# Optimization experiments

Hardware: AMD Instinct MI355X
Metric: run time of the kernel (lower is better)

## Reference

```python
import jax, jax.numpy as jnp
import numpy as np

# Config (mirrors MarketBDHConfig / BDHConfig defaults used here)
B, T = 2, 512
NUM_ASSETS, IN_FEAT = 93, 4
D = 256          # n_embd
NH = 4           # n_head
MULT = 64        # mlp_internal_dim_multiplier
NL = 6           # n_layer
NI = D * MULT // NH  # per-head internal dim N = 4096
IN_DIM = NUM_ASSETS * IN_FEAT  # 372
ROPE_THETA = 2.0 ** 16
EPS = 1e-5


def _ln(x):
    # LayerNorm over last dim, elementwise_affine=False
    m = jnp.mean(x, axis=-1, keepdims=True)
    v = jnp.mean(jnp.square(x - m), axis=-1, keepdims=True)
    return (x - m) * jax.lax.rsqrt(v + EPS)


def _rope(x, cos, sin):
    # x: [B,NH,T,NI]; cos/sin: [T, NI//2] (broadcast over B,NH)
    x1, x2 = x[..., 0::2], x[..., 1::2]
    out = jnp.stack([x1 * cos - x2 * sin, x1 * sin + x2 * cos], axis=-1)
    return out.reshape(x.shape)


def setup_inputs() -> dict:
    key = jax.random.key(0)
    ks = jax.random.split(key, 9)
    s = 0.02
    return {
        "x": jax.random.normal(ks[0], (B, T, NUM_ASSETS, IN_FEAT), jnp.float32),
        "in_W": jax.random.normal(ks[1], (IN_DIM, D), jnp.float32) * s,
        "in_b": jnp.zeros((D,), jnp.float32),
        "encoder": jax.random.normal(ks[2], (NH, D, NI), jnp.float32) * s,
        "encoder_v": jax.random.normal(ks[3], (NH, D, NI), jnp.float32) * s,
        "decoder": jax.random.normal(ks[4], (NH * NI, D), jnp.float32) * s,
        "head_W": jax.random.normal(ks[5], (D, IN_DIM), jnp.float32) * s,
        "head_b": jnp.zeros((IN_DIM,), jnp.float32),
    }


def reference(x, in_W, in_b, encoder, encoder_v, decoder, head_W, head_b):
    # input projection: [B,T,N,F] -> [B,T,IN_DIM] -> [B,T,D]
    x_flat = x.reshape(B, T, IN_DIM)
    h = _ln(x_flat @ in_W + in_b)  # [B,T,D]

    # RoPE phase tables over the internal (latent) dimension
    freqs = 1.0 / (ROPE_THETA ** (jnp.arange(0, NI, 2, dtype=jnp.float32) / NI))
    phases = jnp.arange(T, dtype=jnp.float32)[:, None] * freqs[None, :]  # [T, NI/2]
    cos, sin = jnp.cos(phases), jnp.sin(phases)

    dec = decoder.reshape(NH, NI, D)  # head-major flatten matches transpose(1,2).reshape

    for _ in range(NL):
        h_res = h
        # encode + relu-sparsify: [B,NH,T,NI]
        h_sparse = jax.nn.relu(jnp.einsum('btd,hdn->bhtn', h, encoder))
        # BDH attention: linear (no softmax), K is Q, is_causal=False -> dense scores
        qr = _rope(h_sparse, cos, sin)
        scores = jnp.einsum('bhtn,bhsn->bhts', qr, qr)  # [B,NH,T,T]
        yKV = jnp.einsum('bhts,bsd->bhtd', scores, h)    # V = h broadcast over heads
        yKV = _ln(yKV)
        y_sparse = jax.nn.relu(jnp.einsum('bhtd,hdn->bhtn', yKV, encoder_v))
        xy_sparse = h_sparse * y_sparse  # multiplicative gating (dropout p=0)
        yMLP = jnp.einsum('bhtn,hnd->btd', xy_sparse, dec)
        h = _ln(h_res + _ln(yMLP))

    pred = (h @ head_W + head_b).reshape(B, T, NUM_ASSETS, IN_FEAT)
    return pred
```

## Files before the change

kernel.cpp:

```cpp
#include <hip/hip_runtime.h>
#include <math.h>

#define B_ 2
#define T_ 512
#define D_ 256
#define NH_ 4
#define NI_ 4096
#define IN_DIM_ 372
#define NL_ 6
#define EPS_ 1e-5f

typedef unsigned short u16;
typedef __attribute__((ext_vector_type(4))) float f32x4;
typedef __attribute__((ext_vector_type(8))) short bf16x8;

__device__ __forceinline__ u16 f2b(float f) {
  union { float f; unsigned u; } v; v.f = f;
  unsigned r = v.u + 0x7fffu + ((v.u >> 16) & 1u);
  return (u16)(r >> 16);
}
__device__ __forceinline__ float b2f(u16 s) {
  union { unsigned u; float f; } v; v.u = ((unsigned)s) << 16;
  return v.f;
}

__device__ __forceinline__ void gload16(const u16* g, u16* l) {
  __builtin_amdgcn_global_load_lds(
      (const __attribute__((address_space(1))) unsigned int*)g,
      (__attribute__((address_space(3))) unsigned int*)l, 16, 0, 0);
}

__device__ __forceinline__ float waveSum(float v) {
  #pragma unroll
  for (int o = 32; o > 0; o >>= 1) v += __shfl_xor(v, o, 64);
  return v;
}

__device__ __forceinline__ float blkSum256(float v, float* sb4) {
  #pragma unroll
  for (int o = 32; o > 0; o >>= 1) v += __shfl_down(v, o, 64);
  int w = threadIdx.x >> 6;
  __syncthreads();
  if ((threadIdx.x & 63) == 0) sb4[w] = v;
  __syncthreads();
  return sb4[0] + sb4[1] + sb4[2] + sb4[3];
}

__device__ __forceinline__ void gemm128(const u16* __restrict__ A,
                                        const u16* __restrict__ Bt,
                                        int lda, int k0, int k1,
                                        int row0, int col0,
                                        u16* Als, u16* Bls,
                                        f32x4 acc[4][4]) {
  const int tid = threadIdx.x;
  const int lane = tid & 63;
  const int wv = tid >> 6;
  const int wr = (wv >> 1) << 6;
  const int wc = (wv & 1) << 6;
  const int frow = lane & 15;
  const int kg = lane >> 4;
  const int sw = frow & 7;
  #pragma unroll
  for (int m = 0; m < 4; m++)
    #pragma unroll
    for (int n = 0; n < 4; n++) {
      f32x4 z = {0.f, 0.f, 0.f, 0.f};
      acc[m][n] = z;
    }
  auto stage = [&](int k, int buf) {
    #pragma unroll
    for (int i = 0; i < 4; i++) {
      int s = tid + (i << 8);
      int r = s >> 3;
      int c = (((s & 7) ^ (r & 7)) << 3);
      gload16(A + (long)(row0 + r) * lda + k + c, Als + buf * 8192 + s * 8);
      gload16(Bt + (long)(col0 + r) * lda + k + c, Bls + buf * 8192 + s * 8);
    }
  };
  stage(k0, 0);
  __syncthreads();
  int cur = 0;
  for (int k = k0; k < k1; k += 64) {
    if (k + 64 < k1) stage(k + 64, cur ^ 1);
    const u16* Ab = Als + cur * 8192;
    const u16* Bb = Bls + cur * 8192;
    #pragma unroll
    for (int kk = 0; kk < 2; kk++) {
      const int slot = ((((kk << 2) + kg) ^ sw) << 3);
      bf16x8 af[4], bfv[4];
      #pragma unroll
      for (int m = 0; m < 4; m++)
        af[m] = *(const bf16x8*)(Ab + (wr + m * 16 + frow) * 64 + slot);
      #pragma unroll
      for (int n = 0; n < 4; n++)
        bfv[n] = *(const bf16x8*)(Bb + (wc + n * 16 + frow) * 64 + slot);
      #pragma unroll
      for (int m = 0; m < 4; m++)
        #pragma unroll
        for (int n = 0; n < 4; n++)
          acc[m][n] = __builtin_amdgcn_mfma_f32_16x16x32_bf16(af[m], bfv[n], acc[m][n], 0, 0, 0);
    }
    __syncthreads();
    cur ^= 1;
  }
}

#define EPILOG_SETUP \
  const int lane = threadIdx.x & 63; \
  const int wv = threadIdx.x >> 6; \
  const int wr = (wv >> 1) << 6, wc = (wv & 1) << 6;

#define STAGE_HALF(EXPR) \
  if (wr == h * 64) { \
    _Pragma("unroll") \
    for (int m = 0; m < 4; m++) \
      _Pragma("unroll") \
      for (int n = 0; n < 4; n++) \
        _Pragma("unroll") \
        for (int r = 0; r < 4; r++) { \
          int lr = m * 16 + ((lane >> 4) << 2) + r; \
          int lc = wc + n * 16 + (lane & 15); \
          float _a = acc[m][n][r]; \
          smem[lr * 128 + (lc ^ (((lr >> 2) & 7) << 3))] = f2b(EXPR); \
        } \
  } \
  __syncthreads();

__device__ __forceinline__ void storeC_lds(const f32x4 acc[4][4], u16* smem,
                                           u16* Cb, int ldc, int row0, int col0,
                                           int wr, int wc, int lane) {
  const int tid = threadIdx.x;
  #pragma unroll
  for (int h = 0; h < 2; h++) {
    STAGE_HALF(_a)
    #pragma unroll
    for (int i = 0; i < 4; i++) {
      int idx = i * 256 + tid;
      int lr = idx >> 4, ch = idx & 15;
      uint4 v = *(const uint4*)(smem + lr * 128 + ((ch ^ ((lr >> 2) & 7)) << 3));
      *(uint4*)(Cb + (long)(row0 + h * 64 + lr) * ldc + col0 + ch * 8) = v;
    }
    __syncthreads();
  }
}

__global__ __launch_bounds__(256)
void k_cs(unsigned* __restrict__ cs) {
  int idx = blockIdx.x * 256 + threadIdx.x;
  if (idx >= T_ * (NI_ / 2)) return;
  int t = idx >> 11;
  int k = idx & 2047;
  float freq = exp2f(-(float)k * (1.0f / 128.0f));
  float ph = (float)t * freq;
  cs[idx] = (unsigned)f2b(cosf(ph)) | ((unsigned)f2b(sinf(ph)) << 16);
}

__global__ __launch_bounds__(256)
void ktr(const float* __restrict__ src, u16* __restrict__ dst, int R, int C) {
  __shared__ float tile[64][65];
  long zoff = (long)blockIdx.z * R * C;
  int r0 = blockIdx.y * 64, c0 = blockIdx.x * 64;
  int tid = threadIdx.x;
  int tr = tid >> 4, tc4 = (tid & 15) * 4;
  #pragma unroll
  for (int i = 0; i < 4; i++) {
    int r = tr + i * 16;
    f32x4 v = *(const f32x4*)(src + zoff + (long)(r0 + r) * C + c0 + tc4);
    tile[r][tc4 + 0] = v.x; tile[r][tc4 + 1] = v.y;
    tile[r][tc4 + 2] = v.z; tile[r][tc4 + 3] = v.w;
  }
  __syncthreads();
  #pragma unroll
  for (int i = 0; i < 4; i++) {
    int c = tr + i * 16;
    ushort4 o;
    o.x = f2b(tile[tc4 + 0][c]); o.y = f2b(tile[tc4 + 1][c]);
    o.z = f2b(tile[tc4 + 2][c]); o.w = f2b(tile[tc4 + 3][c]);
    *(ushort4*)(dst + zoff + (long)(c0 + c) * R + r0 + tc4) = o;
  }
}

__global__ __launch_bounds__(256)
void ktrW(const float* __restrict__ e0, const float* __restrict__ e1,
          u16* __restrict__ d0, u16* __restrict__ d1) {
  __shared__ float tile[64][65];
  int z = blockIdx.z;
  const float* src = (z < 4) ? e0 : e1;
  u16* dst = (z < 4) ? d0 : d1;
  long zoff = (long)(z & 3) * D_ * NI_;
  int r0 = blockIdx.y * 64, c0 = blockIdx.x * 64;
  int tid = threadIdx.x;
  int tr = tid >> 4, tc4 = (tid & 15) * 4;
  #pragma unroll
  for (int i = 0; i < 4; i++) {
    int r = tr + i * 16;
    f32x4 v = *(const f32x4*)(src + zoff + (long)(r0 + r) * NI_ + c0 + tc4);
    tile[r][tc4 + 0] = v.x; tile[r][tc4 + 1] = v.y;
    tile[r][tc4 + 2] = v.z; tile[r][tc4 + 3] = v.w;
  }
  __syncthreads();
  #pragma unroll
  for (int i = 0; i < 4; i++) {
    int c = tr + i * 16;
    ushort4 o;
    o.x = f2b(tile[tc4 + 0][c]); o.y = f2b(tile[tc4 + 1][c]);
    o.z = f2b(tile[tc4 + 2][c]); o.w = f2b(tile[tc4 + 3][c]);
    *(ushort4*)(dst + zoff + (long)(c0 + c) * D_ + r0 + tc4) = o;
  }
}

__global__ __launch_bounds__(256)
void k_input(const float* __restrict__ x, const float* __restrict__ W,
             const float* __restrict__ b, float* __restrict__ hf,
             u16* __restrict__ hbf, u16* __restrict__ hT) {
  __shared__ float xr[IN_DIM_];
  __shared__ float sb[4];
  int bt = blockIdx.x;
  int d = threadIdx.x;
  const float* xrow = x + (long)bt * IN_DIM_;
  for (int k = d; k < IN_DIM_; k += 256) xr[k] = xrow[k];
  __syncthreads();
  float acc = b[d];
  for (int k = 0; k < IN_DIM_; k++) acc += xr[k] * W[k * D_ + d];
  float mean = blkSum256(acc, sb) * (1.0f / D_);
  float c = acc - mean;
  float var = blkSum256(c * c, sb) * (1.0f / D_);
  float out = c * rsqrtf(var + EPS_);
  hf[(long)bt * D_ + d] = out;
  hbf[(long)bt * D_ + d] = f2b(out);
  hT[((long)(bt >> 9) * D_ + d) * T_ + (bt & 511)] = f2b(out);
}

__global__ __launch_bounds__(256)
void g_enc(const u16* __restrict__ hbf, const u16* __restrict__ enct,
           const unsigned* __restrict__ cs, u16* __restrict__ qr) {
  __shared__ u16 smem[32768];
  int head = blockIdx.z;
  int row0 = blockIdx.y * 128, col0 = blockIdx.x * 128;
  f32x4 acc[4][4];
  gemm128(hbf, enct + (long)head * NI_ * D_, D_, 0, D_, row0, col0,
          smem, smem + 16384, acc);
  EPILOG_SETUP
  const int tid = threadIdx.x;
  #pragma unroll
  for (int h = 0; h < 2; h++) {
    STAGE_HALF(fmaxf(_a, 0.f))
    #pragma unroll
    for (int i = 0; i < 4; i++) {
      int idx = i * 256 + tid;
      int lr = idx >> 4, ch = idx & 15;
      uint4 v = *(const uint4*)(smem + lr * 128 + ((ch ^ ((lr >> 2) & 7)) << 3));
      int gr = row0 + h * 64 + lr;
      int b = gr >> 9, t = gr & 511;
      int gcol = col0 + ch * 8;
      uint4 csv = *(const uint4*)(cs + (long)t * (NI_ / 2) + (gcol >> 1));
      const unsigned* pv = &v.x; const unsigned* pc = &csv.x;
      unsigned o[4];
      #pragma unroll
      for (int j = 0; j < 4; j++) {
        float v0 = b2f((u16)pv[j]), v1 = b2f((u16)(pv[j] >> 16));
        float cc = b2f((u16)pc[j]), ss = b2f((u16)(pc[j] >> 16));
        o[j] = (unsigned)f2b(v0 * cc - v1 * ss) | ((unsigned)f2b(v0 * ss + v1 * cc) << 16);
      }
      long qri = (((long)(b * NH_ + head)) * T_ + t) * NI_ + gcol;
      *(uint4*)(qr + qri) = make_uint4(o[0], o[1], o[2], o[3]);
    }
    __syncthreads();
  }
}

__global__ __launch_bounds__(256)
void g_scores(const u16* __restrict__ qr, u16* __restrict__ scpb) {
  __shared__ u16 smem[32768];
  int tix = blockIdx.x;
  int by = (tix < 4) ? 0 : (tix < 7) ? 1 : (tix < 9) ? 2 : 3;
  int sub = (by == 0) ? 0 : (by == 1) ? 3 : (by == 2) ? 5 : 6;
  int bx = tix - sub;
  int z2 = blockIdx.z;
  int z = z2 >> 2, ks = z2 & 3;
  const u16* A = qr + (long)z * T_ * NI_;
  int row0 = by * 128, col0 = bx * 128;
  f32x4 acc[4][4];
  gemm128(A, A, NI_, ks * 1024, ks * 1024 + 1024, row0, col0,
          smem, smem + 16384, acc);
  EPILOG_SETUP
  u16* Cb = scpb + (long)(ks * 8 + z) * T_ * T_;
  storeC_lds(acc, smem, Cb, T_, row0, col0, wr, wc, lane);
  if (by != bx) {
    #pragma unroll
    for (int m = 0; m < 4; m++)
      #pragma unroll
      for (int n = 0; n < 4; n++) {
        int gc = col0 + wc + n * 16 + (lane & 15);
        int gr0 = row0 + wr + m * 16 + ((lane >> 4) << 2);
        uint2 o;
        o.x = (unsigned)f2b(acc[m][n][0]) | ((unsigned)f2b(acc[m][n][1]) << 16);
        o.y = (unsigned)f2b(acc[m][n][2]) | ((unsigned)f2b(acc[m][n][3]) << 16);
        *(uint2*)(Cb + (long)gc * T_ + gr0) = o;
      }
  }
}

__global__ __launch_bounds__(256)
void g_ykv(const u16* __restrict__ scpb, const u16* __restrict__ hT,
           u16* __restrict__ ykvpb) {
  __shared__ u16 smem[16384];
  u16* Als = smem;
  u16* Bls = smem + 8192;
  int z2 = blockIdx.z;
  int z = z2 >> 2, ks = z2 & 3;
  int b = z >> 2;
  int row0 = blockIdx.y * 128, col0 = blockIdx.x * 128;
  const long SL = (long)8 * T_ * T_;
  const u16* Ab = scpb + (long)z * T_ * T_;
  const u16* Bt = hT + (long)b * D_ * T_;
  const int tid = threadIdx.x;
  const int lane = tid & 63;
  const int wv = tid >> 6;
  const int wr = (wv >> 1) << 6, wc = (wv & 1) << 6;
  const int frow = lane & 15;
  const int kg = lane >> 4;
  const int sw = frow & 7;
  f32x4 acc[4][4];
  #pragma unroll
  for (int m = 0; m < 4; m++)
    #pragma unroll
    for (int n = 0; n < 4; n++) {
      f32x4 zz = {0.f, 0.f, 0.f, 0.f};
      acc[m][n] = zz;
    }
  const int ar = tid >> 1;
  const int ac0 = (tid & 1) << 2;
  for (int k = ks * 128; k < ks * 128 + 128; k += 64) {
    long gb = (long)(row0 + ar) * T_ + k;
    #pragma unroll
    for (int j = 0; j < 4; j++) {
      int jj = ac0 + j;
      long ga = gb + (jj << 3);
      uint4 p0 = *(const uint4*)(Ab + ga);
      uint4 p1 = *(const uint4*)(Ab + SL + ga);
      uint4 p2 = *(const uint4*)(Ab + 2 * SL + ga);
      uint4 p3 = *(const uint4*)(Ab + 3 * SL + ga);
      const unsigned* q0 = &p0.x; const unsigned* q1 = &p1.x;
      const unsigned* q2 = &p2.x; const unsigned* q3 = &p3.x;
      unsigned o[4];
      #pragma unroll
      for (int w = 0; w < 4; w++) {
        float lo = b2f((u16)q0[w]) + b2f((u16)q1[w]) + b2f((u16)q2[w]) + b2f((u16)q3[w]);
        float hi = b2f((u16)(q0[w] >> 16)) + b2f((u16)(q1[w] >> 16)) +
                   b2f((u16)(q2[w] >> 16)) + b2f((u16)(q3[w] >> 16));
        o[w] = (unsigned)f2b(lo) | ((unsigned)f2b(hi) << 16);
      }
      *(uint4*)(Als + ar * 64 + ((jj ^ (ar & 7)) << 3)) = make_uint4(o[0], o[1], o[2], o[3]);
    }
    #pragma unroll
    for (int i = 0; i < 4; i++) {
      int s = tid + (i << 8);
      int r = s >> 3;
      int c = (((s & 7) ^ (r & 7)) << 3);
      gload16(Bt + (long)(col0 + r) * T_ + k + c, Bls + s * 8);
    }
    __syncthreads();
    #pragma unroll
    for (int kk = 0; kk < 2; kk++) {
      const int slot = ((((kk << 2) + kg) ^ sw) << 3);
      bf16x8 af[4], bfv[4];
      #pragma unroll
      for (int m = 0; m < 4; m++)
        af[m] = *(const bf16x8*)(Als + (wr + m * 16 + frow) * 64 + slot);
      #pragma unroll
      for (int n = 0; n < 4; n++)
        bfv[n] = *(const bf16x8*)(Bls + (wc + n * 16 + frow) * 64 + slot);
      #pragma unroll
      for (int m = 0; m < 4; m++)
        #pragma unroll
        for (int n = 0; n < 4; n++)
          acc[m][n] = __builtin_amdgcn_mfma_f32_16x16x32_bf16(af[m], bfv[n], acc[m][n], 0, 0, 0);
    }
    __syncthreads();
  }
  storeC_lds(acc, smem, ykvpb + (long)(ks * 8 + z) * T_ * D_, D_, row0, col0, wr, wc, lane);
}

__global__ __launch_bounds__(256)
void k_lnykv(const u16* __restrict__ ykvpb, u16* __restrict__ ykvb) {
  int row = blockIdx.x * 4 + (threadIdx.x >> 6);
  int lane = threadIdx.x & 63;
  const long SL = (long)8 * T_ * D_;
  long base = (long)row * D_ + lane * 4;
  float v0 = 0.f, v1 = 0.f, v2 = 0.f, v3 = 0.f;
  #pragma unroll
  for (int p = 0; p < 4; p++) {
    uint2 w = *(const uint2*)(ykvpb + p * SL + base);
    v0 += b2f((u16)w.x); v1 += b2f((u16)(w.x >> 16));
    v2 += b2f((u16)w.y); v3 += b2f((u16)(w.y >> 16));
  }
  float mean = waveSum(v0 + v1 + v2 + v3) * (1.0f / D_);
  float c0 = v0 - mean, c1 = v1 - mean, c2 = v2 - mean, c3 = v3 - mean;
  float var = waveSum(c0 * c0 + c1 * c1 + c2 * c2 + c3 * c3) * (1.0f / D_);
  float rs = rsqrtf(var + EPS_);
  uint2 o;
  o.x = (unsigned)f2b(c0 * rs) | ((unsigned)f2b(c1 * rs) << 16);
  o.y = (unsigned)f2b(c2 * rs) | ((unsigned)f2b(c3 * rs) << 16);
  *(uint2*)(ykvb + base) = o;
}

__global__ __launch_bounds__(256)
void g_ysp(const u16* __restrict__ ykvb, const u16* __restrict__ encvt,
           const u16* __restrict__ qr, const unsigned* __restrict__ cs,
           u16* __restrict__ xy) {
  __shared__ u16 smem[32768];
  int z = blockIdx.z;
  int b = z >> 2, head = z & 3;
  int row0 = blockIdx.y * 128, col0 = blockIdx.x * 128;
  f32x4 acc[4][4];
  gemm128(ykvb + (long)z * T_ * D_, encvt + (long)head * NI_ * D_, D_,
          0, D_, row0, col0, smem, smem + 16384, acc);
  EPILOG_SETUP
  const int tid = threadIdx.x;
  #pragma unroll
  for (int h = 0; h < 2; h++) {
    STAGE_HALF(fmaxf(_a, 0.f))
    #pragma unroll
    for (int i = 0; i < 4; i++) {
      int idx = i * 256 + tid;
      int lr = idx >> 4, ch = idx & 15;
      uint4 v = *(const uint4*)(smem + lr * 128 + ((ch ^ ((lr >> 2) & 7)) << 3));
      int t = row0 + h * 64 + lr;
      int gcol = col0 + ch * 8;
      uint4 qv = *(const uint4*)(qr + ((long)z * T_ + t) * NI_ + gcol);
      uint4 csv = *(const uint4*)(cs + (long)t * (NI_ / 2) + (gcol >> 1));
      const unsigned* pv = &v.x; const unsigned* pq = &qv.x; const unsigned* pc = &csv.x;
      unsigned o[4];
      #pragma unroll
      for (int j = 0; j < 4; j++) {
        float v0 = b2f((u16)pv[j]), v1 = b2f((u16)(pv[j] >> 16));
        float q0 = b2f((u16)pq[j]), q1 = b2f((u16)(pq[j] >> 16));
        float cc = b2f((u16)pc[j]), ss = b2f((u16)(pc[j] >> 16));
        float hs0 = fmaxf(cc * q0 + ss * q1, 0.f);
        float hs1 = fmaxf(cc * q1 - ss * q0, 0.f);
        o[j] = (unsigned)f2b(hs0 * v0) | ((unsigned)f2b(hs1 * v1) << 16);
      }
      long xyi = ((long)b * T_ + t) * (NH_ * NI_) + head * NI_ + gcol;
      *(uint4*)(xy + xyi) = make_uint4(o[0], o[1], o[2], o[3]);
    }
    __syncthreads();
  }
}

__global__ __launch_bounds__(256)
void g_ymlp(const u16* __restrict__ xy, const u16* __restrict__ dect,
            u16* __restrict__ ymlppb) {
  __shared__ u16 smem[32768];
  int ks = blockIdx.z;
  int row0 = blockIdx.y * 128, col0 = blockIdx.x * 128;
  f32x4 acc[4][4];
  gemm128(xy, dect, NH_ * NI_, ks * 1024, ks * 1024 + 1024, row0, col0,
          smem, smem + 16384, acc);
  EPILOG_SETUP
  storeC_lds(acc, smem, ymlppb + (long)ks * (B_ * T_) * D_, D_, row0, col0, wr, wc, lane);
}

__global__ __launch_bounds__(256)
void k_dln(const u16* __restrict__ ymlppb, float* __restrict__ hf,
           u16* __restrict__ hbf, u16* __restrict__ hT) {
  int bt = blockIdx.x * 4 + (threadIdx.x >> 6);
  int lane = threadIdx.x & 63;
  const long SL = (long)(B_ * T_) * D_;
  long base = (long)bt * D_ + lane * 4;
  float v0 = 0.f, v1 = 0.f, v2 = 0.f, v3 = 0.f;
  #pragma unroll
  for (int p = 0; p < 16; p++) {
    uint2 w = *(const uint2*)(ymlppb + p * SL + base);
    v0 += b2f((u16)w.x); v1 += b2f((u16)(w.x >> 16));
    v2 += b2f((u16)w.y); v3 += b2f((u16)(w.y >> 16));
  }
  float mean = waveSum(v0 + v1 + v2 + v3) * (1.0f / D_);
  float c0 = v0 - mean, c1 = v1 - mean, c2 = v2 - mean, c3 = v3 - mean;
  float var = waveSum(c0 * c0 + c1 * c1 + c2 * c2 + c3 * c3) * (1.0f / D_);
  float rs = rsqrtf(var + EPS_);
  f32x4 hv = *(const f32x4*)(hf + base);
  float w0 = hv.x + c0 * rs, w1 = hv.y + c1 * rs;
  float w2 = hv.z + c2 * rs, w3 = hv.w + c3 * rs;
  float m2 = waveSum(w0 + w1 + w2 + w3) * (1.0f / D_);
  float e0 = w0 - m2, e1 = w1 - m2, e2 = w2 - m2, e3 = w3 - m2;
  float va2 = waveSum(e0 * e0 + e1 * e1 + e2 * e2 + e3 * e3) * (1.0f / D_);
  float rs2 = rsqrtf(va2 + EPS_);
  float o0 = e0 * rs2, o1 = e1 * rs2, o2 = e2 * rs2, o3 = e3 * rs2;
  f32x4 of = {o0, o1, o2, o3};
  *(f32x4*)(hf + base) = of;
  uint2 ob;
  ob.x = (unsigned)f2b(o0) | ((unsigned)f2b(o1) << 16);
  ob.y = (unsigned)f2b(o2) | ((unsigned)f2b(o3) << 16);
  *(uint2*)(hbf + base) = ob;
  int b = bt >> 9, t = bt & 511;
  int d0 = lane * 4;
  hT[((long)b * D_ + d0 + 0) * T_ + t] = f2b(o0);
  hT[((long)b * D_ + d0 + 1) * T_ + t] = f2b(o1);
  hT[((long)b * D_ + d0 + 2) * T_ + t] = f2b(o2);
  hT[((long)b * D_ + d0 + 3) * T_ + t] = f2b(o3);
}

__global__ __launch_bounds__(384)
void k_head(const float* __restrict__ h, const float* __restrict__ W,
            const float* __restrict__ bb, float* __restrict__ out) {
  __shared__ float hr[D_];
  int bt = blockIdx.x;
  int j = threadIdx.x;
  for (int k = j; k < D_; k += 384) hr[k] = h[(long)bt * D_ + k];
  __syncthreads();
  if (j < IN_DIM_) {
    float acc = bb[j];
    for (int d2 = 0; d2 < D_; d2++) acc += hr[d2] * W[(long)d2 * IN_DIM_ + j];
    out[(long)bt * IN_DIM_ + j] = acc;
  }
}

extern "C" void kernel_launch(void* const* d_in, const int* in_sizes, int n_in,
                              void* d_out, int out_size, void* d_ws, size_t ws_size,
                              hipStream_t stream) {
  const float* x    = (const float*)d_in[0];
  const float* in_W = (const float*)d_in[1];
  const float* in_b = (const float*)d_in[2];
  const float* enc  = (const float*)d_in[3];
  const float* encv = (const float*)d_in[4];
  const float* dec  = (const float*)d_in[5];
  const float* hW   = (const float*)d_in[6];
  const float* hb   = (const float*)d_in[7];
  float* out = (float*)d_out;

  char* p = (char*)d_ws;
  auto alloc = [&](size_t bytes) { char* r = p; p += (bytes + 255) & ~(size_t)255; return r; };
  unsigned* cs   = (unsigned*)alloc((size_t)T_ * (NI_ / 2) * 4);
  float* hf      = (float*)alloc((size_t)B_ * T_ * D_ * 4);
  u16*   hbf     = (u16*)  alloc((size_t)B_ * T_ * D_ * 2);
  u16*   hT      = (u16*)  alloc((size_t)B_ * D_ * T_ * 2);
  u16*   enct    = (u16*)  alloc((size_t)NH_ * D_ * NI_ * 2);
  u16*   encvt   = (u16*)  alloc((size_t)NH_ * D_ * NI_ * 2);
  u16*   dect    = (u16*)  alloc((size_t)NH_ * NI_ * D_ * 2);
  u16*   qr      = (u16*)  alloc((size_t)B_ * NH_ * T_ * NI_ * 2);
  u16*   xy      = (u16*)  alloc((size_t)B_ * T_ * NH_ * NI_ * 2);
  u16*   scpb    = (u16*)  alloc((size_t)4 * 8 * T_ * T_ * 2);
  u16*   ykvpb   = (u16*)  alloc((size_t)4 * 8 * T_ * D_ * 2);
  u16*   ykvb    = (u16*)  alloc((size_t)8 * T_ * D_ * 2);
  u16*   ymlppb  = (u16*)  alloc((size_t)16 * B_ * T_ * D_ * 2);

  k_cs<<<dim3(4096), dim3(256), 0, stream>>>(cs);
  ktrW<<<dim3(NI_ / 64, D_ / 64, 8), dim3(256), 0, stream>>>(enc, encv, enct, encvt);
  ktr<<<dim3(D_ / 64, (NH_ * NI_) / 64, 1), dim3(256), 0, stream>>>(dec, dect, NH_ * NI_, D_);
  k_input<<<dim3(B_ * T_), dim3(256), 0, stream>>>(x, in_W, in_b, hf, hbf, hT);

  for (int l = 0; l < NL_; l++) {
    g_enc<<<dim3(32, 8, 4), dim3(256), 0, stream>>>(hbf, enct, cs, qr);
    g_scores<<<dim3(10, 1, 32), dim3(256), 0, stream>>>(qr, scpb);
    g_ykv<<<dim3(2, 4, 32), dim3(256), 0, stream>>>(scpb, hT, ykvpb);
    k_lnykv<<<dim3(1024), dim3(256), 0, stream>>>(ykvpb, ykvb);
    g_ysp<<<dim3(32, 4, 8), dim3(256), 0, stream>>>(ykvb, encvt, qr, cs, xy);
    g_ymlp<<<dim3(2, 8, 16), dim3(256), 0, stream>>>(xy, dect, ymlppb);
    k_dln<<<dim3(256), dim3(256), 0, stream>>>(ymlppb, hf, hbf, hT);
  }

  k_head<<<dim3(B_ * T_), dim3(384), 0, stream>>>(hf, hW, hb, out);
}
```

Baseline: 766.3 us.

## Triple-buffer GEMM K-loop with vmcnt waits, dedupe diagonal score loads, batch rows

Replaces the double-buffered 64-wide K-step GEMM core with a triple-buffered 32-wide K-step pipeline. It synchronises with explicit vmcnt waits and raw barriers, and raises wave priority around the MFMA block. Diagonal score tiles load the shared operand only once, and the epilogues now stage the full 128x128 tile in one pass instead of two halves. The input and head projection kernels now process 8 rows per block so each weight load is reused across them. The aim is to hide global-to-LDS latency and reduce LDS footprint and barrier count, at the cost of more K iterations and fragile manual waitcnt accounting.

```diff
diff --git a/kernel.cpp b/kernel.cpp
--- a/kernel.cpp
+++ b/kernel.cpp
@@ -30,6 +30,8 @@
       (__attribute__((address_space(3))) unsigned int*)l, 16, 0, 0);
 }
 
+#define WAITV(N) asm volatile("s_waitcnt vmcnt(" #N ")" ::: "memory")
+
 __device__ __forceinline__ float waveSum(float v) {
   #pragma unroll
   for (int o = 32; o > 0; o >>= 1) v += __shfl_xor(v, o, 64);
@@ -46,12 +48,12 @@
   return sb4[0] + sb4[1] + sb4[2] + sb4[3];
 }
 
-__device__ __forceinline__ void gemm128(const u16* __restrict__ A,
-                                        const u16* __restrict__ Bt,
-                                        int lda, int k0, int k1,
-                                        int row0, int col0,
-                                        u16* Als, u16* Bls,
-                                        f32x4 acc[4][4]) {
+template <int SAMEAB>
+__device__ __forceinline__ void gemm128p(const u16* __restrict__ A,
+                                         const u16* __restrict__ Bt,
+                                         int lda, int k0, int k1,
+                                         int row0, int col0,
+                                         u16* smem, f32x4 acc[4][4]) {
   const int tid = threadIdx.x;
   const int lane = tid & 63;
   const int wv = tid >> 6;
@@ -59,7 +61,8 @@
   const int wc = (wv & 1) << 6;
   const int frow = lane & 15;
   const int kg = lane >> 4;
-  const int sw = frow & 7;
+  u16* Als = smem;
+  u16* Bls = smem + 12288;
   #pragma unroll
   for (int m = 0; m < 4; m++)
     #pragma unroll
@@ -69,46 +72,94 @@
     }
   auto stage = [&](int k, int buf) {
     #pragma unroll
-    for (int i = 0; i < 4; i++) {
+    for (int i = 0; i < 2; i++) {
       int s = tid + (i << 8);
-      int r = s >> 3;
-      int c = (((s & 7) ^ (r & 7)) << 3);
-      gload16(A + (long)(row0 + r) * lda + k + c, Als + buf * 8192 + s * 8);
-      gload16(Bt + (long)(col0 + r) * lda + k + c, Bls + buf * 8192 + s * 8);
+      int r = s >> 2;
+      int c = (((s & 3) ^ (r & 3)) << 3);
+      gload16(A + (long)(row0 + r) * lda + k + c, Als + buf * 4096 + s * 8);
+    }
+    if (!SAMEAB) {
+      #pragma unroll
+      for (int i = 0; i < 2; i++) {
+        int s = tid + (i << 8);
+        int r = s >> 2;
+        int c = (((s & 3) ^ (r & 3)) << 3);
+        gload16(Bt + (long)(col0 + r) * lda + k + c, Bls + buf * 4096 + s * 8);
+      }
     }
   };
+  const int nk = (k1 - k0) >> 5;
   stage(k0, 0);
-  __syncthreads();
-  int cur = 0;
-  for (int k = k0; k < k1; k += 64) {
-    if (k + 64 < k1) stage(k + 64, cur ^ 1);
-    const u16* Ab = Als + cur * 8192;
-    const u16* Bb = Bls + cur * 8192;
-    #pragma unroll
-    for (int kk = 0; kk < 2; kk++) {
-      const int slot = ((((kk << 2) + kg) ^ sw) << 3);
-      bf16x8 af[4], bfv[4];
-      #pragma unroll
-      for (int m = 0; m < 4; m++)
-        af[m] = *(const bf16x8*)(Ab + (wr + m * 16 + frow) * 64 + slot);
+  stage(k0 + 32, 1);
+  for (int i = 0; i < nk; i++) {
+    if (i + 2 < nk) {
+      if (SAMEAB) WAITV(2); else WAITV(4);
+      __builtin_amdgcn_s_barrier();
+      stage(k0 + (i + 2) * 32, (i + 2) % 3);
+    } else if (i + 1 < nk) {
+      if (SAMEAB) WAITV(2); else WAITV(4);
+      __builtin_amdgcn_s_barrier();
+    } else {
+      WAITV(0);
+      __builtin_amdgcn_s_barrier();
+    }
+    const int bi = i % 3;
+    const u16* Ab = Als + bi * 4096;
+    const u16* Bb = SAMEAB ? Ab : (Bls + bi * 4096);
+    bf16x8 af[4], bfv[4];
+    #pragma unroll
+    for (int m = 0; m < 4; m++) {
+      int rr = wr + m * 16 + frow;
+      af[m] = *(const bf16x8*)(Ab + rr * 32 + ((kg ^ (rr & 3)) << 3));
+    }
+    #pragma unroll
+    for (int n = 0; n < 4; n++) {
+      int rr = wc + n * 16 + frow;
+      bfv[n] = *(const bf16x8*)(Bb + rr * 32 + ((kg ^ (rr & 3)) << 3));
+    }
+    __builtin_amdgcn_s_setprio(1);
+    #pragma unroll
+    for (int m = 0; m < 4; m++)
       #pragma unroll
       for (int n = 0; n < 4; n++)
-        bfv[n] = *(const bf16x8*)(Bb + (wc + n * 16 + frow) * 64 + slot);
-      #pragma unroll
-      for (int m = 0; m < 4; m++)
-        #pragma unroll
-        for (int n = 0; n < 4; n++)
-          acc[m][n] = __builtin_amdgcn_mfma_f32_16x16x32_bf16(af[m], bfv[n], acc[m][n], 0, 0, 0);
-    }
-    __syncthreads();
-    cur ^= 1;
-  }
+        acc[m][n] = __builtin_amdgcn_mfma_f32_16x16x32_bf16(af[m], bfv[n], acc[m][n], 0, 0, 0);
+    __builtin_amdgcn_s_setprio(0);
+  }
+  __syncthreads();
 }
 
 #define EPILOG_SETUP \
   const int lane = threadIdx.x & 63; \
   const int wv = threadIdx.x >> 6; \
   const int wr = (wv >> 1) << 6, wc = (wv & 1) << 6;
+
+#define STAGE_FULL(EXPR) \
+  _Pragma("unroll") \
+  for (int m = 0; m < 4; m++) \
+    _Pragma("unroll") \
+    for (int n = 0; n < 4; n++) \
+      _Pragma("unroll") \
+      for (int r = 0; r < 4; r++) { \
+        int lr = wr + m * 16 + ((lane >> 4) << 2) + r; \
+        int lc = wc + n * 16 + (lane & 15); \
+        float _a = acc[m][n][r]; \
+        smem[lr * 128 + (lc ^ (((lr >> 2) & 7) << 3))] = f2b(EXPR); \
+      } \
+  __syncthreads();
+
+__device__ __forceinline__ void storeC_full(const f32x4 acc[4][4], u16* smem,
+                                            u16* Cb, int ldc, int row0, int col0,
+                                            int wr, int wc, int lane) {
+  const int tid = threadIdx.x;
+  STAGE_FULL(_a)
+  #pragma unroll
+  for (int i = 0; i < 8; i++) {
+    int idx = i * 256 + tid;
+    int lr = idx >> 4, ch = idx & 15;
+    uint4 v = *(const uint4*)(smem + lr * 128 + ((ch ^ ((lr >> 2) & 7)) << 3));
+    *(uint4*)(Cb + (long)(row0 + lr) * ldc + col0 + ch * 8) = v;
+  }
+}
 
 #define STAGE_HALF(EXPR) \
   if (wr == h * 64) { \
@@ -213,65 +264,71 @@
 void k_input(const float* __restrict__ x, const float* __restrict__ W,
              const float* __restrict__ b, float* __restrict__ hf,
              u16* __restrict__ hbf, u16* __restrict__ hT) {
-  __shared__ float xr[IN_DIM_];
+  __shared__ float xr[8][IN_DIM_];
   __shared__ float sb[4];
-  int bt = blockIdx.x;
+  int bt0 = blockIdx.x * 8;
   int d = threadIdx.x;
-  const float* xrow = x + (long)bt * IN_DIM_;
-  for (int k = d; k < IN_DIM_; k += 256) xr[k] = xrow[k];
-  __syncthreads();
-  float acc = b[d];
-  for (int k = 0; k < IN_DIM_; k++) acc += xr[k] * W[k * D_ + d];
-  float mean = blkSum256(acc, sb) * (1.0f / D_);
-  float c = acc - mean;
-  float var = blkSum256(c * c, sb) * (1.0f / D_);
-  float out = c * rsqrtf(var + EPS_);
-  hf[(long)bt * D_ + d] = out;
-  hbf[(long)bt * D_ + d] = f2b(out);
-  hT[((long)(bt >> 9) * D_ + d) * T_ + (bt & 511)] = f2b(out);
+  for (int i = d; i < 8 * IN_DIM_; i += 256)
+    xr[i / IN_DIM_][i % IN_DIM_] = x[(long)bt0 * IN_DIM_ + i];
+  __syncthreads();
+  float acc[8];
+  float bias = b[d];
+  #pragma unroll
+  for (int r = 0; r < 8; r++) acc[r] = bias;
+  for (int k = 0; k < IN_DIM_; k++) {
+    float w = W[k * D_ + d];
+    #pragma unroll
+    for (int r = 0; r < 8; r++) acc[r] += xr[r][k] * w;
+  }
+  #pragma unroll
+  for (int r = 0; r < 8; r++) {
+    int bt = bt0 + r;
+    float mean = blkSum256(acc[r], sb) * (1.0f / D_);
+    float c = acc[r] - mean;
+    float var = blkSum256(c * c, sb) * (1.0f / D_);
+    float out = c * rsqrtf(var + EPS_);
+    hf[(long)bt * D_ + d] = out;
+    hbf[(long)bt * D_ + d] = f2b(out);
+    hT[((long)(bt >> 9) * D_ + d) * T_ + (bt & 511)] = f2b(out);
+  }
 }
 
 __global__ __launch_bounds__(256)
 void g_enc(const u16* __restrict__ hbf, const u16* __restrict__ enct,
            const unsigned* __restrict__ cs, u16* __restrict__ qr) {
-  __shared__ u16 smem[32768];
+  __shared__ u16 smem[24576];
   int head = blockIdx.z;
   int row0 = blockIdx.y * 128, col0 = blockIdx.x * 128;
   f32x4 acc[4][4];
-  gemm128(hbf, enct + (long)head * NI_ * D_, D_, 0, D_, row0, col0,
-          smem, smem + 16384, acc);
+  gemm128p<0>(hbf, enct + (long)head * NI_ * D_, D_, 0, D_, row0, col0, smem, acc);
   EPILOG_SETUP
   const int tid = threadIdx.x;
-  #pragma unroll
-  for (int h = 0; h < 2; h++) {
-    STAGE_HALF(fmaxf(_a, 0.f))
-    #pragma unroll
-    for (int i = 0; i < 4; i++) {
-      int idx = i * 256 + tid;
-      int lr = idx >> 4, ch = idx & 15;
-      uint4 v = *(const uint4*)(smem + lr * 128 + ((ch ^ ((lr >> 2) & 7)) << 3));
-      int gr = row0 + h * 64 + lr;
-      int b = gr >> 9, t = gr & 511;
-      int gcol = col0 + ch * 8;
-      uint4 csv = *(const uint4*)(cs + (long)t * (NI_ / 2) + (gcol >> 1));
-      const unsigned* pv = &v.x; const unsigned* pc = &csv.x;
-      unsigned o[4];
-      #pragma unroll
-      for (int j = 0; j < 4; j++) {
-        float v0 = b2f((u16)pv[j]), v1 = b2f((u16)(pv[j] >> 16));
-        float cc = b2f((u16)pc[j]), ss = b2f((u16)(pc[j] >> 16));
-        o[j] = (unsigned)f2b(v0 * cc - v1 * ss) | ((unsigned)f2b(v0 * ss + v1 * cc) << 16);
-      }
-      long qri = (((long)(b * NH_ + head)) * T_ + t) * NI_ + gcol;
-      *(uint4*)(qr + qri) = make_uint4(o[0], o[1], o[2], o[3]);
-    }
-    __syncthreads();
+  STAGE_FULL(fmaxf(_a, 0.f))
+  #pragma unroll
+  for (int i = 0; i < 8; i++) {
+    int idx = i * 256 + tid;
+    int lr = idx >> 4, ch = idx & 15;
+    uint4 v = *(const uint4*)(smem + lr * 128 + ((ch ^ ((lr >> 2) & 7)) << 3));
+    int gr = row0 + lr;
+    int b = gr >> 9, t = gr & 511;
+    int gcol = col0 + ch * 8;
+    uint4 csv = *(const uint4*)(cs + (long)t * (NI_ / 2) + (gcol >> 1));
+    const unsigned* pv = &v.x; const unsigned* pc = &csv.x;
+    unsigned o[4];
+    #pragma unroll
+    for (int j = 0; j < 4; j++) {
+      float v0 = b2f((u16)pv[j]), v1 = b2f((u16)(pv[j] >> 16));
+      float cc = b2f((u16)pc[j]), ss = b2f((u16)(pc[j] >> 16));
+      o[j] = (unsigned)f2b(v0 * cc - v1 * ss) | ((unsigned)f2b(v0 * ss + v1 * cc) << 16);
+    }
+    long qri = (((long)(b * NH_ + head)) * T_ + t) * NI_ + gcol;
+    *(uint4*)(qr + qri) = make_uint4(o[0], o[1], o[2], o[3]);
   }
 }
 
 __global__ __launch_bounds__(256)
 void g_scores(const u16* __restrict__ qr, u16* __restrict__ scpb) {
-  __shared__ u16 smem[32768];
+  __shared__ u16 smem[24576];
   int tix = blockIdx.x;
   int by = (tix < 4) ? 0 : (tix < 7) ? 1 : (tix < 9) ? 2 : 3;
   int sub = (by == 0) ? 0 : (by == 1) ? 3 : (by == 2) ? 5 : 6;
@@ -281,11 +338,13 @@
   const u16* A = qr + (long)z * T_ * NI_;
   int row0 = by * 128, col0 = bx * 128;
   f32x4 acc[4][4];
-  gemm128(A, A, NI_, ks * 1024, ks * 1024 + 1024, row0, col0,
-          smem, smem + 16384, acc);
+  if (by == bx)
+    gemm128p<1>(A, A, NI_, ks * 1024, ks * 1024 + 1024, row0, col0, smem, acc);
+  else
+    gemm128p<0>(A, A, NI_, ks * 1024, ks * 1024 + 1024, row0, col0, smem, acc);
   EPILOG_SETUP
   u16* Cb = scpb + (long)(ks * 8 + z) * T_ * T_;
-  storeC_lds(acc, smem, Cb, T_, row0, col0, wr, wc, lane);
+  storeC_full(acc, smem, Cb, T_, row0, col0, wr, wc, lane);
   if (by != bx) {
     #pragma unroll
     for (int m = 0; m < 4; m++)
@@ -371,11 +430,13 @@
       #pragma unroll
       for (int n = 0; n < 4; n++)
         bfv[n] = *(const bf16x8*)(Bls + (wc + n * 16 + frow) * 64 + slot);
+      __builtin_amdgcn_s_setprio(1);
       #pragma unroll
       for (int m = 0; m < 4; m++)
         #pragma unroll
         for (int n = 0; n < 4; n++)
           acc[m][n] = __builtin_amdgcn_mfma_f32_16x16x32_bf16(af[m], bfv[n], acc[m][n], 0, 0, 0);
+      __builtin_amdgcn_s_setprio(0);
     }
     __syncthreads();
   }
@@ -409,56 +470,51 @@
 void g_ysp(const u16* __restrict__ ykvb, const u16* __restrict__ encvt,
            const u16* __restrict__ qr, const unsigned* __restrict__ cs,
            u16* __restrict__ xy) {
-  __shared__ u16 smem[32768];
+  __shared__ u16 smem[24576];
   int z = blockIdx.z;
   int b = z >> 2, head = z & 3;
   int row0 = blockIdx.y * 128, col0 = blockIdx.x * 128;
   f32x4 acc[4][4];
-  gemm128(ykvb + (long)z * T_ * D_, encvt + (long)head * NI_ * D_, D_,
-          0, D_, row0, col0, smem, smem + 16384, acc);
+  gemm128p<0>(ykvb + (long)z * T_ * D_, encvt + (long)head * NI_ * D_, D_,
+              0, D_, row0, col0, smem, acc);
   EPILOG_SETUP
   const int tid = threadIdx.x;
-  #pragma unroll
-  for (int h = 0; h < 2; h++) {
-    STAGE_HALF(fmaxf(_a, 0.f))
-    #pragma unroll
-    for (int i = 0; i < 4; i++) {
-      int idx = i * 256 + tid;
-      int lr = idx >> 4, ch = idx & 15;
-      uint4 v = *(const uint4*)(smem + lr * 128 + ((ch ^ ((lr >> 2) & 7)) << 3));
-      int t = row0 + h * 64 + lr;
-      int gcol = col0 + ch * 8;
-      uint4 qv = *(const uint4*)(qr + ((long)z * T_ + t) * NI_ + gcol);
-      uint4 csv = *(const uint4*)(cs + (long)t * (NI_ / 2) + (gcol >> 1));
-      const unsigned* pv = &v.x; const unsigned* pq = &qv.x; const unsigned* pc = &csv.x;
-      unsigned o[4];
-      #pragma unroll
-      for (int j = 0; j < 4; j++) {
-        float v0 = b2f((u16)pv[j]), v1 = b2f((u16)(pv[j] >> 16));
-        float q0 = b2f((u16)pq[j]), q1 = b2f((u16)(pq[j] >> 16));
-        float cc = b2f((u16)pc[j]), ss = b2f((u16)(pc[j] >> 16));
-        float hs0 = fmaxf(cc * q0 + ss * q1, 0.f);
-        float hs1 = fmaxf(cc * q1 - ss * q0, 0.f);
-        o[j] = (unsigned)f2b(hs0 * v0) | ((unsigned)f2b(hs1 * v1) << 16);
-      }
-      long xyi = ((long)b * T_ + t) * (NH_ * NI_) + head * NI_ + gcol;
-      *(uint4*)(xy + xyi) = make_uint4(o[0], o[1], o[2], o[3]);
-    }
-    __syncthreads();
+  STAGE_FULL(fmaxf(_a, 0.f))
+  #pragma unroll
+  for (int i = 0; i < 8; i++) {
+    int idx = i * 256 + tid;
+    int lr = idx >> 4, ch = idx & 15;
+    uint4 v = *(const uint4*)(smem + lr * 128 + ((ch ^ ((lr >> 2) & 7)) << 3));
+    int t = row0 + lr;
+    int gcol = col0 + ch * 8;
+    uint4 qv = *(const uint4*)(qr + ((long)z * T_ + t) * NI_ + gcol);
+    uint4 csv = *(const uint4*)(cs + (long)t * (NI_ / 2) + (gcol >> 1));
+    const unsigned* pv = &v.x; const unsigned* pq = &qv.x; const unsigned* pc = &csv.x;
+    unsigned o[4];
+    #pragma unroll
+    for (int j = 0; j < 4; j++) {
+      float v0 = b2f((u16)pv[j]), v1 = b2f((u16)(pv[j] >> 16));
+      float q0 = b2f((u16)pq[j]), q1 = b2f((u16)(pq[j] >> 16));
+      float cc = b2f((u16)pc[j]), ss = b2f((u16)(pc[j] >> 16));
+      float hs0 = fmaxf(cc * q0 + ss * q1, 0.f);
+      float hs1 = fmaxf(cc * q1 - ss * q0, 0.f);
+      o[j] = (unsigned)f2b(hs0 * v0) | ((unsigned)f2b(hs1 * v1) << 16);
+    }
+    long xyi = ((long)b * T_ + t) * (NH_ * NI_) + head * NI_ + gcol;
+    *(uint4*)(xy + xyi) = make_uint4(o[0], o[1], o[2], o[3]);
   }
 }
 
 __global__ __launch_bounds__(256)
 void g_ymlp(const u16* __restrict__ xy, const u16* __restrict__ dect,
             u16* __restrict__ ymlppb) {
-  __shared__ u16 smem[32768];
+  __shared__ u16 smem[24576];
   int ks = blockIdx.z;
   int row0 = blockIdx.y * 128, col0 = blockIdx.x * 128;
   f32x4 acc[4][4];
-  gemm128(xy, dect, NH_ * NI_, ks * 1024, ks * 1024 + 1024, row0, col0,
-          smem, smem + 16384, acc);
+  gemm128p<0>(xy, dect, NH_ * NI_, ks * 1024, ks * 1024 + 1024, row0, col0, smem, acc);
   EPILOG_SETUP
-  storeC_lds(acc, smem, ymlppb + (long)ks * (B_ * T_) * D_, D_, row0, col0, wr, wc, lane);
+  storeC_full(acc, smem, ymlppb + (long)ks * (B_ * T_) * D_, D_, row0, col0, wr, wc, lane);
 }
 
 __global__ __launch_bounds__(256)
@@ -504,15 +560,25 @@
 __global__ __launch_bounds__(384)
 void k_head(const float* __restrict__ h, const float* __restrict__ W,
             const float* __restrict__ bb, float* __restrict__ out) {
-  __shared__ float hr[D_];
-  int bt = blockIdx.x;
+  __shared__ float hr[8][D_];
+  int bt0 = blockIdx.x * 8;
   int j = threadIdx.x;
-  for (int k = j; k < D_; k += 384) hr[k] = h[(long)bt * D_ + k];
+  for (int i = j; i < 8 * D_; i += 384)
+    hr[i >> 8][i & 255] = h[(long)bt0 * D_ + i];
   __syncthreads();
   if (j < IN_DIM_) {
-    float acc = bb[j];
-    for (int d2 = 0; d2 < D_; d2++) acc += hr[d2] * W[(long)d2 * IN_DIM_ + j];
-    out[(long)bt * IN_DIM_ + j] = acc;
+    float acc[8];
+    float bias = bb[j];
+    #pragma unroll
+    for (int r = 0; r < 8; r++) acc[r] = bias;
+    for (int d2 = 0; d2 < D_; d2++) {
+      float w = W[(long)d2 * IN_DIM_ + j];
+      #pragma unroll
+      for (int r = 0; r < 8; r++) acc[r] += hr[r][d2] * w;
+    }
+    #pragma unroll
+    for (int r = 0; r < 8; r++)
+      out[(long)(bt0 + r) * IN_DIM_ + j] = acc[r];
   }
 }
 
@@ -548,7 +614,7 @@
   k_cs<<<dim3(4096), dim3(256), 0, stream>>>(cs);
   ktrW<<<dim3(NI_ / 64, D_ / 64, 8), dim3(256), 0, stream>>>(enc, encv, enct, encvt);
   ktr<<<dim3(D_ / 64, (NH_ * NI_) / 64, 1), dim3(256), 0, stream>>>(dec, dect, NH_ * NI_, D_);
-  k_input<<<dim3(B_ * T_), dim3(256), 0, stream>>>(x, in_W, in_b, hf, hbf, hT);
+  k_input<<<dim3(B_ * T_ / 8), dim3(256), 0, stream>>>(x, in_W, in_b, hf, hbf, hT);
 
   for (int l = 0; l < NL_; l++) {
     g_enc<<<dim3(32, 8, 4), dim3(256), 0, stream>>>(hbf, enct, cs, qr);
@@ -560,5 +626,5 @@
     k_dln<<<dim3(256), dim3(256), 0, stream>>>(ymlppb, hf, hbf, hT);
   }
 
-  k_head<<<dim3(B_ * T_), dim3(384), 0, stream>>>(hf, hW, hb, out);
-}
+  k_head<<<dim3(B_ * T_ / 8), dim3(384), 0, stream>>>(hf, hW, hb, out);
+}
```

Result: no change. 754.8 us (-1.5%).
